# Kernel tuning notes

Hardware: AMD Instinct MI355X
Metric: run time of the kernel (lower is better)

Reference implementation:

```python
import jax, jax.numpy as jnp
import numpy as np
from jax import lax

# Mamba hyperparams (mamba_ssm defaults for d_model=768)
D_MODEL = 768
N_LAYER = 8
D_INNER = 2 * D_MODEL          # 1536
D_STATE = 16
DT_RANK = D_MODEL // 16        # 48
D_CONV = 4
BATCH = 4
SEQLEN = 1024


def _ln(x, w, b):
    mu = jnp.mean(x, axis=-1, keepdims=True)
    var = jnp.mean(jnp.square(x - mu), axis=-1, keepdims=True)
    return (x - mu) * lax.rsqrt(var + 1e-5) * w + b


def _silu(x):
    return x * jax.nn.sigmoid(x)


def _mamba_mixer(h, in_proj, conv_w, conv_b, x_proj, dt_w, dt_b, A_log, Dv, out_proj):
    # h: [B, L, d_model]
    xz = jnp.einsum('bld,ed->ble', h, in_proj)          # [B, L, 2*d_inner]
    xm, z = jnp.split(xz, 2, axis=-1)
    # causal depthwise conv1d over time
    xc = lax.conv_general_dilated(
        xm.transpose(0, 2, 1), conv_w, (1,), [(D_CONV - 1, 0)],
        feature_group_count=D_INNER)                    # [B, d_inner, L]
    u = _silu((xc + conv_b[None, :, None]).transpose(0, 2, 1))  # [B, L, d_inner]
    dbc = jnp.einsum('bld,ed->ble', u, x_proj)          # [B, L, dt_rank+2*d_state]
    dt = jax.nn.softplus(jnp.einsum('blr,dr->bld', dbc[..., :DT_RANK], dt_w) + dt_b)
    Bm = dbc[..., DT_RANK:DT_RANK + D_STATE]            # [B, L, d_state]
    Cm = dbc[..., DT_RANK + D_STATE:]                   # [B, L, d_state]
    A = -jnp.exp(A_log)                                 # [d_inner, d_state]

    def step(hstate, inp):
        dt_t, B_t, u_t, C_t = inp                       # [B,d_inner],[B,d_state],[B,d_inner],[B,d_state]
        dA = jnp.exp(dt_t[..., None] * A)               # [B, d_inner, d_state]
        hstate = dA * hstate + (dt_t * u_t)[..., None] * B_t[:, None, :]
        y = jnp.einsum('bds,bs->bd', hstate, C_t)
        return hstate, y

    h0 = jnp.zeros((h.shape[0], D_INNER, D_STATE), h.dtype)
    _, ys = lax.scan(step, h0, (dt.transpose(1, 0, 2), Bm.transpose(1, 0, 2),
                                u.transpose(1, 0, 2), Cm.transpose(1, 0, 2)))
    y = ys.transpose(1, 0, 2) + u * Dv                  # skip connection D*u
    y = y * _silu(z)
    return jnp.einsum('ble,de->bld', y, out_proj)


def setup_inputs() -> dict:
    key = jax.random.key(0)
    ks = jax.random.split(key, 16)
    f32 = jnp.float32
    d = {
        'x': jax.random.normal(ks[0], (BATCH, SEQLEN, D_MODEL), f32),
        'pos': jax.random.normal(ks[1], (BATCH, SEQLEN, D_MODEL), f32),
        'norm_w': jnp.ones((N_LAYER, D_MODEL), f32),
        'norm_b': jnp.zeros((N_LAYER, D_MODEL), f32),
        'in_proj': jax.random.normal(ks[2], (N_LAYER, 2 * D_INNER, D_MODEL), f32) * 0.02,
        'conv_w': jax.random.normal(ks[3], (N_LAYER, D_INNER, 1, D_CONV), f32) * 0.2,
        'conv_b': jnp.zeros((N_LAYER, D_INNER), f32),
        'x_proj': jax.random.normal(ks[4], (N_LAYER, DT_RANK + 2 * D_STATE, D_INNER), f32) * 0.02,
        'dt_w': jax.random.normal(ks[5], (N_LAYER, D_INNER, DT_RANK), f32) * 0.1,
        'dt_b': jax.random.uniform(ks[6], (N_LAYER, D_INNER), f32, -4.0, -2.0),
        'A_log': jnp.broadcast_to(jnp.log(jnp.arange(1, D_STATE + 1, dtype=f32)),
                                  (N_LAYER, D_INNER, D_STATE)).copy(),
        'Dv': jnp.ones((N_LAYER, D_INNER), f32),
        'out_proj': jax.random.normal(ks[7], (N_LAYER, D_MODEL, D_INNER), f32) * 0.02,
        'normf_w': jnp.ones((D_MODEL,), f32),
        'normf_b': jnp.zeros((D_MODEL,), f32),
        'dec_w': jnp.ones((D_MODEL,), f32),
        'dec_b': jnp.zeros((D_MODEL,), f32),
        'return_token_num': 256,
    }
    return d


def reference(x, pos, norm_w, norm_b, in_proj, conv_w, conv_b, x_proj, dt_w, dt_b,
              A_log, Dv, out_proj, normf_w, normf_b, dec_w, dec_b, return_token_num):
    hidden = x + pos
    residual = None
    for l in range(N_LAYER):
        residual = hidden if residual is None else hidden + residual
        h = _ln(residual, norm_w[l], norm_b[l])
        hidden = _mamba_mixer(h, in_proj[l], conv_w[l], conv_b[l], x_proj[l],
                              dt_w[l], dt_b[l], A_log[l], Dv[l], out_proj[l])
    residual = hidden + residual
    hidden = _ln(residual, normf_w, normf_b)
    return _ln(hidden[:, -return_token_num:], dec_w, dec_b)
```

## Files before the change

### kernel.cpp

```cpp
#include <hip/hip_runtime.h>
#include <math.h>

#define D_MODEL 768
#define N_LAYER 8
#define D_INNER 1536
#define D_STATE 16
#define DT_RANK 48
#define D_CONV  4
#define BATCH   4
#define SEQLEN  1024
#define NTOK    (BATCH*SEQLEN)
#define DBC_W   (DT_RANK + 2*D_STATE)
#define NC      64
#define CHUNK_T (SEQLEN/NC)
#define XP_KS   16
#define XP_KSL  (D_INNER/XP_KS)
#define CONV_TCH 16
#define OP_KS   4

typedef __attribute__((ext_vector_type(8))) short short8v;
typedef __attribute__((ext_vector_type(4))) float float4v;

__device__ __forceinline__ void split_bf16(float x, short& hi, short& lo) {
  unsigned u = __float_as_uint(x);
  unsigned r = (u + 0x7fffu + ((u >> 16) & 1u)) >> 16;
  hi = (short)r;
  float fhi = __uint_as_float(r << 16);
  float xl = x - fhi;
  unsigned u2 = __float_as_uint(xl);
  unsigned r2 = (u2 + 0x7fffu + ((u2 >> 16) & 1u)) >> 16;
  lo = (short)r2;
}

__device__ __forceinline__ void gload16(const short* g, short* l) {
  __builtin_amdgcn_global_load_lds(
      (const __attribute__((address_space(1))) void*)g,
      (__attribute__((address_space(3))) void*)l, 16, 0, 0);
}

__global__ __launch_bounds__(256) void split_kernel(
    const float* __restrict__ src, short* __restrict__ hi,
    short* __restrict__ lo, int n4) {
  int stride = gridDim.x * 256;
  for (int i = blockIdx.x * 256 + threadIdx.x; i < n4; i += stride) {
    float4 v = ((const float4*)src)[i];
    short4 h, g;
    split_bf16(v.x, h.x, g.x);
    split_bf16(v.y, h.y, g.y);
    split_bf16(v.z, h.z, g.z);
    split_bf16(v.w, h.w, g.w);
    ((short4*)hi)[i] = h;
    ((short4*)lo)[i] = g;
  }
}

__global__ __launch_bounds__(256) void ln_kernel(
    const float* __restrict__ x, const float* __restrict__ pos,
    float* __restrict__ resid, const float* __restrict__ opart,
    short* __restrict__ hh_hi, short* __restrict__ hh_lo,
    const float* __restrict__ w, const float* __restrict__ b, int first) {
  int row = blockIdx.x;
  int tid = threadIdx.x;
  size_t base4 = (size_t)row * (D_MODEL / 4);
  __shared__ float red[256];
  __shared__ float s_mu, s_rs;
  float4 v = make_float4(0.f, 0.f, 0.f, 0.f);
  bool act = tid < D_MODEL / 4;
  if (act) {
    if (first) {
      float4 a = ((const float4*)x)[base4 + tid];
      float4 p = ((const float4*)pos)[base4 + tid];
      v = make_float4(a.x + p.x, a.y + p.y, a.z + p.z, a.w + p.w);
    } else {
      float4 r = ((const float4*)resid)[base4 + tid];
      float4 o = ((const float4*)opart)[base4 + tid];
      float4 s = make_float4(o.x, o.y, o.z, o.w);
#pragma unroll
      for (int k = 1; k < OP_KS; ++k) {
        float4 o2 = ((const float4*)opart)[(size_t)k * (NTOK * D_MODEL / 4) + base4 + tid];
        s.x += o2.x; s.y += o2.y; s.z += o2.z; s.w += o2.w;
      }
      v = make_float4(r.x + s.x, r.y + s.y, r.z + s.z, r.w + s.w);
    }
    ((float4*)resid)[base4 + tid] = v;
  }
  red[tid] = act ? (v.x + v.y + v.z + v.w) : 0.f;
  __syncthreads();
  for (int off = 128; off > 0; off >>= 1) {
    if (tid < off) red[tid] += red[tid + off];
    __syncthreads();
  }
  if (tid == 0) s_mu = red[0] / D_MODEL;
  __syncthreads();
  float mu = s_mu;
  float q = 0.f;
  if (act) {
    float dx = v.x - mu, dy = v.y - mu, dz = v.z - mu, dw = v.w - mu;
    q = dx * dx + dy * dy + dz * dz + dw * dw;
  }
  __syncthreads();
  red[tid] = q; __syncthreads();
  for (int off = 128; off > 0; off >>= 1) {
    if (tid < off) red[tid] += red[tid + off];
    __syncthreads();
  }
  if (tid == 0) s_rs = rsqrtf(red[0] / D_MODEL + 1e-5f);
  __syncthreads();
  float rs = s_rs;
  if (act) {
    float4 wv = ((const float4*)w)[tid];
    float4 bv = ((const float4*)b)[tid];
    float o0 = (v.x - mu) * rs * wv.x + bv.x;
    float o1 = (v.y - mu) * rs * wv.y + bv.y;
    float o2 = (v.z - mu) * rs * wv.z + bv.z;
    float o3 = (v.w - mu) * rs * wv.w + bv.w;
    short4 h, g;
    split_bf16(o0, h.x, g.x); split_bf16(o1, h.y, g.y);
    split_bf16(o2, h.z, g.z); split_bf16(o3, h.w, g.w);
    ((short4*)hh_hi)[base4 + tid] = h;
    ((short4*)hh_lo)[base4 + tid] = g;
  }
}

__global__ __launch_bounds__(256) void gemm_bf16x3(
    const short* __restrict__ Ahi, const short* __restrict__ Alo, int lda,
    const short* __restrict__ Bhi, const short* __restrict__ Blo, int ldb,
    float* __restrict__ C, int M, int N, int K) {
  const int BK = 32;
  __shared__ short Ash[128][32];
  __shared__ short Asl[128][32];
  __shared__ short Bsh[128][32];
  __shared__ short Bsl[128][32];
  int brow = blockIdx.y * 128;
  int bcol = blockIdx.x * 128;
  int ksl = K / gridDim.z;
  int kbeg = blockIdx.z * ksl;
  int kend = kbeg + ksl;
  float* Cw = C + (size_t)blockIdx.z * M * N;
  int tid = threadIdx.x;
  int wv = tid >> 6, l = tid & 63;
  int wr = (wv >> 1) * 64;
  int wc = (wv & 1) * 64;
  int lrow = l & 15;
  int rslot = ((l >> 4) ^ ((l >> 1) & 3)) * 8;
  int lr = l >> 2;
  int lp = l & 3;
  float4v zero = {0.f, 0.f, 0.f, 0.f};
  float4v acc[4][4];
#pragma unroll
  for (int m = 0; m < 4; ++m)
#pragma unroll
    for (int n = 0; n < 4; ++n) acc[m][n] = zero;

  for (int k0 = kbeg; k0 < kend; k0 += BK) {
#pragma unroll
    for (int half = 0; half < 2; ++half) {
      int row = wv * 32 + half * 16 + lr;
      int s = lp ^ ((row >> 1) & 3);
      int ldsrow = wv * 32 + half * 16;
      size_t ao = (size_t)(brow + row) * lda + k0 + s * 8;
      size_t bo = (size_t)(bcol + row) * ldb + k0 + s * 8;
      gload16(Ahi + ao, &Ash[ldsrow][0]);
      gload16(Alo + ao, &Asl[ldsrow][0]);
      gload16(Bhi + bo, &Bsh[ldsrow][0]);
      gload16(Blo + bo, &Bsl[ldsrow][0]);
    }
    __syncthreads();
    short8v ah[4], al[4];
#pragma unroll
    for (int m = 0; m < 4; ++m) {
      int R = wr + m * 16 + lrow;
      ah[m] = *(const short8v*)&Ash[R][rslot];
      al[m] = *(const short8v*)&Asl[R][rslot];
    }
#pragma unroll
    for (int n = 0; n < 4; ++n) {
      int R = wc + n * 16 + lrow;
      short8v bh = *(const short8v*)&Bsh[R][rslot];
      short8v bl = *(const short8v*)&Bsl[R][rslot];
#pragma unroll
      for (int m = 0; m < 4; ++m) {
        acc[m][n] = __builtin_amdgcn_mfma_f32_16x16x32_bf16(ah[m], bh, acc[m][n], 0, 0, 0);
        acc[m][n] = __builtin_amdgcn_mfma_f32_16x16x32_bf16(ah[m], bl, acc[m][n], 0, 0, 0);
        acc[m][n] = __builtin_amdgcn_mfma_f32_16x16x32_bf16(al[m], bh, acc[m][n], 0, 0, 0);
      }
    }
    __syncthreads();
  }
  int drow = (l >> 4) * 4, dcol = l & 15;
#pragma unroll
  for (int m = 0; m < 4; ++m)
#pragma unroll
    for (int n = 0; n < 4; ++n)
#pragma unroll
      for (int j = 0; j < 4; ++j)
        Cw[(size_t)(brow + wr + m * 16 + drow + j) * N + bcol + wc + n * 16 + dcol] =
            acc[m][n][j];
}

__global__ __launch_bounds__(256) void xproj_gemm(
    const float* __restrict__ u, const float* __restrict__ xp,
    float* __restrict__ part) {
  const int BM = 64, BK = 32;
  __shared__ __align__(16) float As[BK][BM + 4];
  __shared__ float Bs[BK][DBC_W + 1];
  int brow = blockIdx.x * BM;
  int kbase = blockIdx.y * XP_KSL;
  int tid = threadIdx.x;
  int tr = (tid / 16) * 4;
  int tc = (tid % 16) * 5;
  float acc[4][5] = {};
  for (int k0 = kbase; k0 < kbase + XP_KSL; k0 += BK) {
#pragma unroll
    for (int it = 0; it < 2; ++it) {
      int lin = tid + it * 256;
      int r  = lin >> 3;
      int kq = (lin & 7) * 4;
      float4 a = *(const float4*)&u[(size_t)(brow + r) * D_INNER + k0 + kq];
      As[kq + 0][r] = a.x; As[kq + 1][r] = a.y;
      As[kq + 2][r] = a.z; As[kq + 3][r] = a.w;
    }
#pragma unroll
    for (int it = 0; it < 3; ++it) {
      int lin = tid + it * 256;
      if (lin < 640) {
        int e  = lin >> 3;
        int kq = (lin & 7) * 4;
        float4 bv = *(const float4*)&xp[(size_t)e * D_INNER + k0 + kq];
        Bs[kq + 0][e] = bv.x; Bs[kq + 1][e] = bv.y;
        Bs[kq + 2][e] = bv.z; Bs[kq + 3][e] = bv.w;
      }
    }
    __syncthreads();
#pragma unroll
    for (int kk = 0; kk < BK; ++kk) {
      float4 av = *(const float4*)&As[kk][tr];
      float ar[4] = {av.x, av.y, av.z, av.w};
      float br[5];
#pragma unroll
      for (int j = 0; j < 5; ++j) br[j] = Bs[kk][tc + j];
#pragma unroll
      for (int i = 0; i < 4; ++i)
#pragma unroll
        for (int j = 0; j < 5; ++j) acc[i][j] += ar[i] * br[j];
    }
    __syncthreads();
  }
  float* dst = part + (size_t)blockIdx.y * NTOK * DBC_W;
#pragma unroll
  for (int i = 0; i < 4; ++i)
#pragma unroll
    for (int j = 0; j < 5; ++j)
      dst[(size_t)(brow + tr + i) * DBC_W + tc + j] = acc[i][j];
}

__global__ __launch_bounds__(256) void reduce_dbc_kernel(
    const float* __restrict__ part, float* __restrict__ dbc, int n4) {
  int i = blockIdx.x * 256 + threadIdx.x;
  if (i >= n4) return;
  float4 s = ((const float4*)part)[i];
#pragma unroll
  for (int k = 1; k < XP_KS; ++k) {
    float4 v = ((const float4*)(part + (size_t)k * NTOK * DBC_W))[i];
    s.x += v.x; s.y += v.y; s.z += v.z; s.w += v.w;
  }
  ((float4*)dbc)[i] = s;
}

__global__ __launch_bounds__(256) void conv_silu_kernel(
    const float* __restrict__ xz, const float* __restrict__ cw,
    const float* __restrict__ cb, float* __restrict__ u) {
  int idx = blockIdx.x * 256 + threadIdx.x;
  const int NTC = SEQLEN / CONV_TCH;
  const int C4 = D_INNER / 4;
  if (idx >= BATCH * NTC * C4) return;
  int c4 = idx % C4;
  int tc = (idx / C4) % NTC;
  int b  = idx / (C4 * NTC);
  int t0 = tc * CONV_TCH;
  int c = c4 * 4;
  float4 w0 = ((const float4*)cw)[c + 0];
  float4 w1 = ((const float4*)cw)[c + 1];
  float4 w2 = ((const float4*)cw)[c + 2];
  float4 w3 = ((const float4*)cw)[c + 3];
  float4 bias = ((const float4*)cb)[c4];
  const float4* base = (const float4*)(xz + (size_t)b * SEQLEN * (2 * D_INNER)) + c4;
  const int STR = 2 * D_INNER / 4;
  float4 xm3 = make_float4(0.f, 0.f, 0.f, 0.f);
  float4 xm2 = xm3, xm1 = xm3;
  if (t0 > 0) {
    xm3 = base[(size_t)(t0 - 3) * STR];
    xm2 = base[(size_t)(t0 - 2) * STR];
    xm1 = base[(size_t)(t0 - 1) * STR];
  }
  float4* ub = (float4*)(u + (size_t)(b * SEQLEN + t0) * D_INNER) + c4;
  const int USTR = D_INNER / 4;
#pragma unroll
  for (int i = 0; i < CONV_TCH; ++i) {
    float4 xt = base[(size_t)(t0 + i) * STR];
    float4 a;
    a.x = bias.x + xm3.x * w0.x + xm2.x * w0.y + xm1.x * w0.z + xt.x * w0.w;
    a.y = bias.y + xm3.y * w1.x + xm2.y * w1.y + xm1.y * w1.z + xt.y * w1.w;
    a.z = bias.z + xm3.z * w2.x + xm2.z * w2.y + xm1.z * w2.z + xt.z * w2.w;
    a.w = bias.w + xm3.w * w3.x + xm2.w * w3.y + xm1.w * w3.z + xt.w * w3.w;
    float4 o;
    o.x = a.x / (1.f + __expf(-a.x));
    o.y = a.y / (1.f + __expf(-a.y));
    o.z = a.z / (1.f + __expf(-a.z));
    o.w = a.w / (1.f + __expf(-a.w));
    ub[(size_t)i * USTR] = o;
    xm3 = xm2; xm2 = xm1; xm1 = xt;
  }
}

__device__ __forceinline__ float softplusf(float a) {
  return (a > 20.f) ? a : log1pf(__expf(a));
}

__global__ __launch_bounds__(256) void scan_chunk1(
    float* __restrict__ dty, const float* __restrict__ u,
    const float* __restrict__ dbc, const float* __restrict__ A_log,
    const float* __restrict__ dtw, const float* __restrict__ dtb,
    float* __restrict__ S, float* __restrict__ dtsum) {
  int blk = blockIdx.x;
  int bcq = (blk * 256) / D_INNER;
  int d = blk * 256 - bcq * D_INNER + threadIdx.x;
  int c = bcq & (NC - 1);
  int b = bcq / NC;
  float A[D_STATE];
#pragma unroll
  for (int s = 0; s < D_STATE; ++s) A[s] = -__expf(A_log[d * D_STATE + s]);
  float w[DT_RANK];
  {
    const float4* w4 = (const float4*)(dtw + (size_t)d * DT_RANK);
#pragma unroll
    for (int j = 0; j < DT_RANK / 4; ++j) {
      float4 v = w4[j];
      w[j * 4 + 0] = v.x; w[j * 4 + 1] = v.y;
      w[j * 4 + 2] = v.z; w[j * 4 + 3] = v.w;
    }
  }
  float bias = dtb[d];
  float h[D_STATE];
#pragma unroll
  for (int s = 0; s < D_STATE; ++s) h[s] = 0.f;
  float dts = 0.f;
  int t0 = c * CHUNK_T;
  for (int t = t0; t < t0 + CHUNK_T; ++t) {
    size_t rowb = (size_t)b * SEQLEN + t;
    const float* bc = dbc + rowb * DBC_W;
    float raw = bias;
#pragma unroll
    for (int k = 0; k < DT_RANK; ++k) raw += bc[k] * w[k];
    float dtv = softplusf(raw);
    dty[rowb * D_INNER + d] = dtv;
    float uv  = u[rowb * D_INNER + d];
    float dtu = dtv * uv;
    dts += dtv;
#pragma unroll
    for (int s = 0; s < D_STATE; ++s) {
      float da = __expf(dtv * A[s]);
      h[s] = da * h[s] + dtu * bc[DT_RANK + s];
    }
  }
  size_t base = (((size_t)b * NC + c) * D_STATE) * D_INNER + d;
#pragma unroll
  for (int s = 0; s < D_STATE; ++s) S[base + (size_t)s * D_INNER] = h[s];
  dtsum[((size_t)b * NC + c) * D_INNER + d] = dts;
}

__global__ __launch_bounds__(256) void scan_combine(
    float* __restrict__ S, const float* __restrict__ dtsum,
    const float* __restrict__ A_log) {
  int g = blockIdx.x * 256 + threadIdx.x;
  if (g >= BATCH * D_STATE * D_INNER) return;
  int d = g % D_INNER;
  int s = (g / D_INNER) % D_STATE;
  int b = g / (D_INNER * D_STATE);
  float A = -__expf(A_log[d * D_STATE + s]);
  float h = 0.f;
  for (int c = 0; c < NC; ++c) {
    size_t off = (((size_t)b * NC + c) * D_STATE + s) * D_INNER + d;
    float dts = dtsum[((size_t)b * NC + c) * D_INNER + d];
    float Sv = S[off];
    S[off] = h;
    h = __expf(dts * A) * h + Sv;
  }
}

__global__ __launch_bounds__(256) void scan_chunk2(
    const float* __restrict__ dty, const float* __restrict__ u,
    const float* __restrict__ dbc, const float* __restrict__ xz,
    const float* __restrict__ A_log,
    const float* __restrict__ Dv, const float* __restrict__ hin,
    short* __restrict__ y_hi, short* __restrict__ y_lo) {
  int blk = blockIdx.x;
  int bcq = (blk * 256) / D_INNER;
  int d = blk * 256 - bcq * D_INNER + threadIdx.x;
  int c = bcq & (NC - 1);
  int b = bcq / NC;
  float A[D_STATE];
#pragma unroll
  for (int s = 0; s < D_STATE; ++s) A[s] = -__expf(A_log[d * D_STATE + s]);
  float Dval = Dv[d];
  float h[D_STATE];
  size_t hbase = (((size_t)b * NC + c) * D_STATE) * D_INNER + d;
#pragma unroll
  for (int s = 0; s < D_STATE; ++s) h[s] = hin[hbase + (size_t)s * D_INNER];
  int t0 = c * CHUNK_T;
  for (int t = t0; t < t0 + CHUNK_T; ++t) {
    size_t rowb = (size_t)b * SEQLEN + t;
    const float* bc = dbc + rowb * DBC_W;
    float dtv = dty[rowb * D_INNER + d];
    float uv  = u[rowb * D_INNER + d];
    float dtu = dtv * uv;
    float yv = 0.f;
#pragma unroll
    for (int s = 0; s < D_STATE; ++s) {
      float da = __expf(dtv * A[s]);
      h[s] = da * h[s] + dtu * bc[DT_RANK + s];
      yv += h[s] * bc[DT_RANK + D_STATE + s];
    }
    float zv = xz[rowb * (2 * D_INNER) + D_INNER + d];
    float sig = 1.f / (1.f + __expf(-zv));
    float yo = (yv + uv * Dval) * (zv * sig);
    short hv, lv; split_bf16(yo, hv, lv);
    y_hi[rowb * D_INNER + d] = hv;
    y_lo[rowb * D_INNER + d] = lv;
  }
}

__global__ __launch_bounds__(256) void final_kernel(
    const float* __restrict__ opart, const float* __restrict__ resid,
    const float* __restrict__ fw, const float* __restrict__ fb,
    const float* __restrict__ dw, const float* __restrict__ db,
    float* __restrict__ out, int rtn) {
  int rowo = blockIdx.x;
  int b = rowo / rtn;
  int t = SEQLEN - rtn + (rowo % rtn);
  int tid = threadIdx.x;
  size_t base4 = ((size_t)b * SEQLEN + t) * (D_MODEL / 4);
  __shared__ float red[256];
  __shared__ float s_mu1, s_rs1, s_mu2, s_rs2;
  bool act = tid < D_MODEL / 4;
  float4 v = make_float4(0.f, 0.f, 0.f, 0.f);
  if (act) {
    float4 o = ((const float4*)opart)[base4 + tid];
    float4 s = make_float4(o.x, o.y, o.z, o.w);
#pragma unroll
    for (int k = 1; k < OP_KS; ++k) {
      float4 o2 = ((const float4*)opart)[(size_t)k * (NTOK * D_MODEL / 4) + base4 + tid];
      s.x += o2.x; s.y += o2.y; s.z += o2.z; s.w += o2.w;
    }
    float4 r = ((const float4*)resid)[base4 + tid];
    v = make_float4(r.x + s.x, r.y + s.y, r.z + s.z, r.w + s.w);
  }
  red[tid] = act ? (v.x + v.y + v.z + v.w) : 0.f;
  __syncthreads();
  for (int off = 128; off > 0; off >>= 1) {
    if (tid < off) red[tid] += red[tid + off];
    __syncthreads();
  }
  if (tid == 0) s_mu1 = red[0] / D_MODEL;
  __syncthreads();
  float mu = s_mu1, q = 0.f;
  if (act) {
    float dx = v.x - mu, dy = v.y - mu, dz = v.z - mu, dww = v.w - mu;
    q = dx * dx + dy * dy + dz * dz + dww * dww;
  }
  __syncthreads();
  red[tid] = q; __syncthreads();
  for (int off = 128; off > 0; off >>= 1) {
    if (tid < off) red[tid] += red[tid + off];
    __syncthreads();
  }
  if (tid == 0) s_rs1 = rsqrtf(red[0] / D_MODEL + 1e-5f);
  __syncthreads();
  float rs = s_rs1;
  if (act) {
    float4 wv = ((const float4*)fw)[tid];
    float4 bv = ((const float4*)fb)[tid];
    v.x = (v.x - mu) * rs * wv.x + bv.x;
    v.y = (v.y - mu) * rs * wv.y + bv.y;
    v.z = (v.z - mu) * rs * wv.z + bv.z;
    v.w = (v.w - mu) * rs * wv.w + bv.w;
  }
  __syncthreads();
  red[tid] = act ? (v.x + v.y + v.z + v.w) : 0.f;
  __syncthreads();
  for (int off = 128; off > 0; off >>= 1) {
    if (tid < off) red[tid] += red[tid + off];
    __syncthreads();
  }
  if (tid == 0) s_mu2 = red[0] / D_MODEL;
  __syncthreads();
  mu = s_mu2; q = 0.f;
  if (act) {
    float dx = v.x - mu, dy = v.y - mu, dz = v.z - mu, dww = v.w - mu;
    q = dx * dx + dy * dy + dz * dz + dww * dww;
  }
  __syncthreads();
  red[tid] = q; __syncthreads();
  for (int off = 128; off > 0; off >>= 1) {
    if (tid < off) red[tid] += red[tid + off];
    __syncthreads();
  }
  if (tid == 0) s_rs2 = rsqrtf(red[0] / D_MODEL + 1e-5f);
  __syncthreads();
  rs = s_rs2;
  if (act) {
    float4 wv = ((const float4*)dw)[tid];
    float4 bv = ((const float4*)db)[tid];
    float4 o;
    o.x = (v.x - mu) * rs * wv.x + bv.x;
    o.y = (v.y - mu) * rs * wv.y + bv.y;
    o.z = (v.z - mu) * rs * wv.z + bv.z;
    o.w = (v.w - mu) * rs * wv.w + bv.w;
    ((float4*)out)[(size_t)rowo * (D_MODEL / 4) + tid] = o;
  }
}

extern "C" void kernel_launch(void* const* d_in, const int* in_sizes, int n_in,
                              void* d_out, int out_size, void* d_ws, size_t ws_size,
                              hipStream_t stream) {
  const float* x       = (const float*)d_in[0];
  const float* pos     = (const float*)d_in[1];
  const float* norm_w  = (const float*)d_in[2];
  const float* norm_b  = (const float*)d_in[3];
  const float* in_proj = (const float*)d_in[4];
  const float* conv_w  = (const float*)d_in[5];
  const float* conv_b  = (const float*)d_in[6];
  const float* x_proj  = (const float*)d_in[7];
  const float* dt_w    = (const float*)d_in[8];
  const float* dt_b    = (const float*)d_in[9];
  const float* A_log   = (const float*)d_in[10];
  const float* Dv      = (const float*)d_in[11];
  const float* out_proj= (const float*)d_in[12];
  const float* normf_w = (const float*)d_in[13];
  const float* normf_b = (const float*)d_in[14];
  const float* dec_w   = (const float*)d_in[15];
  const float* dec_b   = (const float*)d_in[16];
  int rtn = out_size / (BATCH * D_MODEL);

  const size_t WI = (size_t)2 * D_INNER * D_MODEL;
  const size_t WO = (size_t)D_MODEL * D_INNER;

  float* ws    = (float*)d_ws;
  float* resid = ws;
  float* xz    = resid + (size_t)NTOK * D_MODEL;
  float* u     = xz    + (size_t)NTOK * 2 * D_INNER;
  float* dbc   = u     + (size_t)NTOK * D_INNER;
  float* dty   = dbc   + (size_t)NTOK * DBC_W;
  float* Sbuf  = dty   + (size_t)NTOK * D_INNER;
  float* dtsum = Sbuf  + (size_t)BATCH * NC * D_STATE * D_INNER;
  float* dbcp  = Sbuf;
  short* hh_hi = (short*)(dtsum + (size_t)BATCH * NC * D_INNER);
  short* hh_lo = hh_hi + (size_t)NTOK * D_MODEL;
  short* y_hi  = hh_lo + (size_t)NTOK * D_MODEL;
  short* y_lo  = y_hi  + (size_t)NTOK * D_INNER;
  short* wIh   = y_lo  + (size_t)NTOK * D_INNER;
  short* wIl   = wIh + N_LAYER * WI;
  short* wOh   = wIl + N_LAYER * WI;
  short* wOl   = wOh + N_LAYER * WO;
  float* opart = xz;

  split_kernel<<<2048, 256, 0, stream>>>(in_proj, wIh, wIl,
                                         (int)(N_LAYER * WI / 4));
  split_kernel<<<2048, 256, 0, stream>>>(out_proj, wOh, wOl,
                                         (int)(N_LAYER * WO / 4));

  for (int l = 0; l < N_LAYER; ++l) {
    ln_kernel<<<NTOK, 256, 0, stream>>>(x, pos, resid, opart, hh_hi, hh_lo,
        norm_w + l * D_MODEL, norm_b + l * D_MODEL, l == 0);

    dim3 g1(2 * D_INNER / 128, NTOK / 128, 1);
    gemm_bf16x3<<<g1, 256, 0, stream>>>(hh_hi, hh_lo, D_MODEL,
        wIh + l * WI, wIl + l * WI, D_MODEL, xz, NTOK, 2 * D_INNER, D_MODEL);

    int convtot = BATCH * (SEQLEN / CONV_TCH) * (D_INNER / 4);
    conv_silu_kernel<<<(convtot + 255) / 256, 256, 0, stream>>>(
        xz, conv_w + (size_t)l * D_INNER * D_CONV, conv_b + l * D_INNER, u);

    dim3 gxp(NTOK / 64, XP_KS);
    xproj_gemm<<<gxp, 256, 0, stream>>>(
        u, x_proj + (size_t)l * DBC_W * D_INNER, dbcp);
    reduce_dbc_kernel<<<(NTOK * DBC_W / 4 + 255) / 256, 256, 0, stream>>>(
        dbcp, dbc, NTOK * DBC_W / 4);

    const float* Al = A_log + (size_t)l * D_INNER * D_STATE;
    const float* dtwl = dt_w + (size_t)l * D_INNER * DT_RANK;
    const float* dtbl = dt_b + (size_t)l * D_INNER;
    int tot1 = BATCH * NC * D_INNER;
    scan_chunk1<<<tot1 / 256, 256, 0, stream>>>(
        dty, u, dbc, Al, dtwl, dtbl, Sbuf, dtsum);
    scan_combine<<<(BATCH * D_STATE * D_INNER + 255) / 256, 256, 0, stream>>>(
        Sbuf, dtsum, Al);
    scan_chunk2<<<tot1 / 256, 256, 0, stream>>>(
        dty, u, dbc, xz, Al, Dv + l * D_INNER, Sbuf, y_hi, y_lo);

    dim3 g2(D_MODEL / 128, NTOK / 128, OP_KS);
    gemm_bf16x3<<<g2, 256, 0, stream>>>(y_hi, y_lo, D_INNER,
        wOh + l * WO, wOl + l * WO, D_INNER, opart, NTOK, D_MODEL, D_INNER);
  }

  final_kernel<<<BATCH * rtn, 256, 0, stream>>>(
      opart, resid, normf_w, normf_b, dec_w, dec_b, (float*)d_out, rtn);
}
```

Before: 2.135 ms.

## Compute local scan outputs in first pass and apply carry-in correction separately

The first chunked-scan pass now produces the intra-chunk output (including the D*u skip) from a zero initial state. It overwrites u in place and stores the cumulative dt within each chunk. The second pass no longer reruns the recurrence. It adds the carried-in state contribution C·(h_in·exp(cumdt·A)) per state element and applies the gate. This removes the duplicated sequential recurrence and the B loads from the second pass. In exchange the first pass gains the C dot product and an extra store, and u is clobbered after the scan.

```diff
diff --git a/kernel.cpp b/kernel.cpp
--- a/kernel.cpp
+++ b/kernel.cpp
@@ -318,9 +318,10 @@
 }
 
 __global__ __launch_bounds__(256) void scan_chunk1(
-    float* __restrict__ dty, const float* __restrict__ u,
+    float* __restrict__ cdt, float* uy,
     const float* __restrict__ dbc, const float* __restrict__ A_log,
     const float* __restrict__ dtw, const float* __restrict__ dtb,
+    const float* __restrict__ Dv,
     float* __restrict__ S, float* __restrict__ dtsum) {
   int blk = blockIdx.x;
   int bcq = (blk * 256) / D_INNER;
@@ -341,6 +342,7 @@
     }
   }
   float bias = dtb[d];
+  float Dval = Dv[d];
   float h[D_STATE];
 #pragma unroll
   for (int s = 0; s < D_STATE; ++s) h[s] = 0.f;
@@ -353,15 +355,18 @@
 #pragma unroll
     for (int k = 0; k < DT_RANK; ++k) raw += bc[k] * w[k];
     float dtv = softplusf(raw);
-    dty[rowb * D_INNER + d] = dtv;
-    float uv  = u[rowb * D_INNER + d];
+    dts += dtv;
+    cdt[rowb * D_INNER + d] = dts;
+    float uv = uy[rowb * D_INNER + d];
     float dtu = dtv * uv;
-    dts += dtv;
+    float yv = 0.f;
 #pragma unroll
     for (int s = 0; s < D_STATE; ++s) {
       float da = __expf(dtv * A[s]);
       h[s] = da * h[s] + dtu * bc[DT_RANK + s];
-    }
+      yv += h[s] * bc[DT_RANK + D_STATE + s];
+    }
+    uy[rowb * D_INNER + d] = yv + uv * Dval;
   }
   size_t base = (((size_t)b * NC + c) * D_STATE) * D_INNER + d;
 #pragma unroll
@@ -388,11 +393,10 @@
   }
 }
 
-__global__ __launch_bounds__(256) void scan_chunk2(
-    const float* __restrict__ dty, const float* __restrict__ u,
+__global__ __launch_bounds__(256) void scan_fix(
+    const float* __restrict__ cdt, const float* __restrict__ uy,
     const float* __restrict__ dbc, const float* __restrict__ xz,
-    const float* __restrict__ A_log,
-    const float* __restrict__ Dv, const float* __restrict__ hin,
+    const float* __restrict__ A_log, const float* __restrict__ hin,
     short* __restrict__ y_hi, short* __restrict__ y_lo) {
   int blk = blockIdx.x;
   int bcq = (blk * 256) / D_INNER;
@@ -402,28 +406,22 @@
   float A[D_STATE];
 #pragma unroll
   for (int s = 0; s < D_STATE; ++s) A[s] = -__expf(A_log[d * D_STATE + s]);
-  float Dval = Dv[d];
-  float h[D_STATE];
+  float hC[D_STATE];
   size_t hbase = (((size_t)b * NC + c) * D_STATE) * D_INNER + d;
 #pragma unroll
-  for (int s = 0; s < D_STATE; ++s) h[s] = hin[hbase + (size_t)s * D_INNER];
+  for (int s = 0; s < D_STATE; ++s) hC[s] = hin[hbase + (size_t)s * D_INNER];
   int t0 = c * CHUNK_T;
   for (int t = t0; t < t0 + CHUNK_T; ++t) {
     size_t rowb = (size_t)b * SEQLEN + t;
     const float* bc = dbc + rowb * DBC_W;
-    float dtv = dty[rowb * D_INNER + d];
-    float uv  = u[rowb * D_INNER + d];
-    float dtu = dtv * uv;
-    float yv = 0.f;
-#pragma unroll
-    for (int s = 0; s < D_STATE; ++s) {
-      float da = __expf(dtv * A[s]);
-      h[s] = da * h[s] + dtu * bc[DT_RANK + s];
-      yv += h[s] * bc[DT_RANK + D_STATE + s];
-    }
+    float cdtv = cdt[rowb * D_INNER + d];
+    float yv = uy[rowb * D_INNER + d];
+#pragma unroll
+    for (int s = 0; s < D_STATE; ++s)
+      yv += bc[DT_RANK + D_STATE + s] * hC[s] * __expf(cdtv * A[s]);
     float zv = xz[rowb * (2 * D_INNER) + D_INNER + d];
     float sig = 1.f / (1.f + __expf(-zv));
-    float yo = (yv + uv * Dval) * (zv * sig);
+    float yo = yv * (zv * sig);
     short hv, lv; split_bf16(yo, hv, lv);
     y_hi[rowb * D_INNER + d] = hv;
     y_lo[rowb * D_INNER + d] = lv;
@@ -550,8 +548,8 @@
   float* xz    = resid + (size_t)NTOK * D_MODEL;
   float* u     = xz    + (size_t)NTOK * 2 * D_INNER;
   float* dbc   = u     + (size_t)NTOK * D_INNER;
-  float* dty   = dbc   + (size_t)NTOK * DBC_W;
-  float* Sbuf  = dty   + (size_t)NTOK * D_INNER;
+  float* cdt   = dbc   + (size_t)NTOK * DBC_W;
+  float* Sbuf  = cdt   + (size_t)NTOK * D_INNER;
   float* dtsum = Sbuf  + (size_t)BATCH * NC * D_STATE * D_INNER;
   float* dbcp  = Sbuf;
   short* hh_hi = (short*)(dtsum + (size_t)BATCH * NC * D_INNER);
@@ -592,11 +590,11 @@
     const float* dtbl = dt_b + (size_t)l * D_INNER;
     int tot1 = BATCH * NC * D_INNER;
     scan_chunk1<<<tot1 / 256, 256, 0, stream>>>(
-        dty, u, dbc, Al, dtwl, dtbl, Sbuf, dtsum);
+        cdt, u, dbc, Al, dtwl, dtbl, Dv + l * D_INNER, Sbuf, dtsum);
     scan_combine<<<(BATCH * D_STATE * D_INNER + 255) / 256, 256, 0, stream>>>(
         Sbuf, dtsum, Al);
-    scan_chunk2<<<tot1 / 256, 256, 0, stream>>>(
-        dty, u, dbc, xz, Al, Dv + l * D_INNER, Sbuf, y_hi, y_lo);
+    scan_fix<<<tot1 / 256, 256, 0, stream>>>(
+        cdt, u, dbc, xz, Al, Sbuf, y_hi, y_lo);
 
     dim3 g2(D_MODEL / 128, NTOK / 128, OP_KS);
     gemm_bf16x3<<<g2, 256, 0, stream>>>(y_hi, y_lo, D_INNER,
```

New measurement: 2.159 ms. About the same (+1.1%).
